# Optimization experiments

Hardware: AMD Instinct MI355X
Metric: run time of the kernel (lower is better)

## Reference

```python
import jax, jax.numpy as jnp
import numpy as np
from jax import lax

N_TAPS = 27  # 3x3x3 kernel

def _gather_one(xb, ti, hi, wi):
    # xb: (C,T,H,W); ti/hi/wi: (T,H,W) int32. Zero-fill outside bounds.
    C, T, H, W = xb.shape
    valid = (ti >= 0) & (ti < T) & (hi >= 0) & (hi < H) & (wi >= 0) & (wi < W)
    lin = (jnp.clip(ti, 0, T - 1) * H + jnp.clip(hi, 0, H - 1)) * W + jnp.clip(wi, 0, W - 1)
    v = jnp.take(xb.reshape(C, -1), lin.reshape(-1), axis=1).reshape(C, T, H, W)
    return v * valid.astype(xb.dtype)

_gather = jax.vmap(_gather_one)  # over batch

def _trilinear(x, t, h, w):
    # x: (B,C,T,H,W); t/h/w: (B,T,H,W) float sample coordinates.
    t0, h0, w0 = jnp.floor(t), jnp.floor(h), jnp.floor(w)
    lt, lh, lw = t - t0, h - h0, w - w0
    t0i, h0i, w0i = t0.astype(jnp.int32), h0.astype(jnp.int32), w0.astype(jnp.int32)
    acc = 0.0
    for ti, wt in ((t0i, 1.0 - lt), (t0i + 1, lt)):
        for hi, wh in ((h0i, 1.0 - lh), (h0i + 1, lh)):
            for wi, ww in ((w0i, 1.0 - lw), (w0i + 1, lw)):
                acc = acc + _gather(x, ti, hi, wi) * (wt * wh * ww)[:, None]
    return acc  # (B,C,T,H,W)

def _deform_conv3d(x, offset_w, offset_b, weight):
    # x: (B,Cin,T,H,W). Offset layout: (B, 3, 27, T, H, W), axis1=(dt,dh,dw),
    # tap index k = kt*9 + kh*3 + kw. stride=1, padding=1, dilation=1, no bias.
    off = lax.conv_general_dilated(
        x, offset_w, (1, 1, 1), [(1, 1)] * 3,
        dimension_numbers=("NCDHW", "OIDHW", "NCDHW"))
    off = off + offset_b[None, :, None, None, None]
    B, _, T, H, W = off.shape
    off = off.reshape(B, 3, N_TAPS, T, H, W)
    tg = jnp.arange(T, dtype=x.dtype)[:, None, None]
    hg = jnp.arange(H, dtype=x.dtype)[None, :, None]
    wg = jnp.arange(W, dtype=x.dtype)[None, None, :]
    out = jnp.zeros((B, weight.shape[0], T, H, W), x.dtype)
    for k in range(N_TAPS):
        kt, kh, kw = k // 9, (k // 3) % 3, k % 3
        t = tg + (kt - 1) + off[:, 0, k]
        h = hg + (kh - 1) + off[:, 1, k]
        w = wg + (kw - 1) + off[:, 2, k]
        s = _trilinear(x, t, h, w)  # (B,Cin,T,H,W)
        out = out + jnp.einsum('bcthw,oc->bothw', s, weight[:, :, kt, kh, kw])
    return out

def setup_inputs() -> dict:
    key = jax.random.key(0)
    ks = jax.random.split(key, 4)
    B, T, C, H, W = 1, 4, 64, 128, 128
    x = jax.random.normal(ks[0], (B, T, C, H, W), jnp.float32)
    # small init scale keeps predicted offsets in a realistic +-2px range
    offset_w = jax.random.normal(ks[1], (3 * N_TAPS, C, 3, 3, 3), jnp.float32) * 0.02
    offset_b = jnp.zeros((3 * N_TAPS,), jnp.float32)
    weight = jax.random.normal(ks[2], (C, C, 3, 3, 3), jnp.float32) * 0.02
    gamma = jax.random.normal(ks[3], (1,), jnp.float32) * 0.1
    return {"x": x, "offset_w": offset_w, "offset_b": offset_b,
            "weight": weight, "gamma": gamma}

def reference(x, offset_w, offset_b, weight, gamma):
    xp = jnp.transpose(x, (0, 2, 1, 3, 4))  # (B,C,T,H,W)
    xc = _deform_conv3d(xp, offset_w, offset_b, weight)
    return gamma[0] * jnp.transpose(xc, (0, 2, 1, 3, 4)) + x
```

## Files before the change

kernel.cpp:

```cpp
#include <hip/hip_runtime.h>
#include <cmath>

#define Cc 64
#define Hh 128
#define Ww 128
#define HW_ 16384
#define THW_ 65536
#define CHW_ 1048576
#define NT 27

typedef unsigned short ushort_t;
typedef _Float16 f16x2 __attribute__((ext_vector_type(2)));
typedef _Float16 f16x8 __attribute__((ext_vector_type(8)));
typedef __fp16 fp16x2_alt __attribute__((ext_vector_type(2)));
typedef float floatx4 __attribute__((ext_vector_type(4)));

union U32H2 { unsigned u; f16x2 h; };

static __device__ inline ushort_t f2h(float f) {
  union { _Float16 h; ushort_t u; } v;
  v.h = (_Float16)f;
  return v.u;
}

static __device__ inline unsigned pk2(float a) {
  union { fp16x2_alt h; unsigned u; } v;
  v.h = __builtin_amdgcn_cvt_pkrtz(a, a);
  return v.u;
}

#if defined(__has_builtin)
#if __has_builtin(__builtin_amdgcn_make_buffer_rsrc) && __has_builtin(__builtin_amdgcn_raw_buffer_load_b32)
#define USE_BUF 1
#endif
#endif
#ifndef USE_BUF
#define USE_BUF 0
#endif

struct XtBuf {
#if USE_BUF
  __amdgpu_buffer_rsrc_t r;
#else
  const unsigned* p;
#endif
};

static __device__ inline XtBuf mkbuf(const ushort_t* xt) {
  XtBuf b;
#if USE_BUF
  b.r = __builtin_amdgcn_make_buffer_rsrc((void*)xt, (short)0, 8388608, 0x00020000);
#else
  b.p = (const unsigned*)xt;
#endif
  return b;
}

static __device__ inline unsigned xload(const XtBuf& b, unsigned voff) {
#if USE_BUF
  return (unsigned)__builtin_amdgcn_raw_buffer_load_b32(b.r, (int)voff, 0, 0);
#else
  return b.p[voff >> 2];
#endif
}


__global__ __launch_bounds__(256) void prep(
    const float* __restrict__ offset_w,
    const float* __restrict__ weight,
    ushort_t* __restrict__ w2frag,
    ushort_t* __restrict__ wfrag)
{
  int e = blockIdx.x * 256 + threadIdx.x;
  if (e < 165888) {
    int j = e & 7, ln = (e >> 3) & 63, kh2 = (e >> 9) & 1, r = e >> 10;
    int ot = r % 6, k = r / 6;
    int oc = ot * 16 + (ln & 15);
    int c  = kh2 * 32 + (ln >> 4) * 8 + j;
    float v = (oc < 81) ? offset_w[(oc * 64 + c) * 27 + k] : 0.f;
    w2frag[e] = f2h(v);
  }
  if (e < 110592) {
    int j = e & 7, ln = (e >> 3) & 63, kh2 = (e >> 9) & 1, r = e >> 10;
    int ot = r & 3, k = r >> 2;
    int o = ot * 16 + (ln & 15);
    int c = kh2 * 32 + (ln >> 4) * 8 + j;
    wfrag[e] = f2h(weight[(o * 64 + c) * 27 + k]);
  }
}

__global__ __launch_bounds__(256) void transpose_x(
    const float* __restrict__ x, ushort_t* __restrict__ xt)
{
  __shared__ float tile[64][65];
  int b = blockIdx.x;
  int wblk = b & 1;
  int th = b >> 1;
  int h = th & 127;
  int t = th >> 7;
  int w0 = wblk * 64;
  int lane = threadIdx.x & 63;
  int quad = threadIdx.x >> 6;
  #pragma unroll
  for (int cc = 0; cc < 16; ++cc) {
    int c = cc * 4 + quad;
    tile[c][lane] = x[t * CHW_ + c * HW_ + h * Ww + w0 + lane];
  }
  __syncthreads();
  #pragma unroll
  for (int ww = 0; ww < 16; ++ww) {
    int w = ww * 4 + quad;
    xt[(size_t)(t * HW_ + h * Ww + w0 + w) * 64 + lane] = f2h(tile[lane][w]);
  }
}

__global__ __launch_bounds__(256) void offconv(
    const ushort_t* __restrict__ xt,
    const ushort_t* __restrict__ w2frag,
    const float* __restrict__ ob,
    float* __restrict__ off)
{
  __shared__ __align__(16) char lds[24960];
  ushort_t* S = (ushort_t*)lds;
  float* Dbuf = (float*)lds;
  int lane = threadIdx.x & 63;
  int wavei = __builtin_amdgcn_readfirstlane(threadIdx.x >> 6);
  int quad = lane >> 4;
  int m16 = lane & 15;
  int hlf = lane >> 5;
  int lo4 = (lane & 31) * 4;
  int p0 = blockIdx.x * 64;
  int t = p0 >> 14;
  int h = (p0 >> 7) & 127;
  int w0 = p0 & 127;
  XtBuf xb = mkbuf(xt);

  floatx4 acc[6];
  #pragma unroll
  for (int i = 0; i < 6; ++i) acc[i] = (floatx4){0.f, 0.f, 0.f, 0.f};

  for (int k = 0; k < NT; ++k) {
    int kt = k / 9, kh = (k / 3) % 3, kw = k % 3;
    int ts = t + kt - 1;
    int hs = h + kh - 1;
    bool rowok = ((unsigned)ts < 4u) && ((unsigned)hs < 128u);
    if (!rowok) continue;
    int sbase = ts * HW_ + hs * Ww;
    #pragma unroll
    for (int j = 0; j < 8; ++j) {
      int prow = wavei * 16 + j * 2 + hlf;
      int wc = w0 + prow + kw - 1;
      bool ok = (unsigned)wc < 128u;
      int wcc = min(max(wc, 0), 127);
      unsigned voff = ((unsigned)(sbase + wcc) << 7) + lo4;
      unsigned d = xload(xb, voff);
      d = ok ? d : 0u;
      *(unsigned*)((char*)S + prow * 144 + lo4) = d;
    }
    const ushort_t* srow = S + (wavei * 16 + m16) * 72 + quad * 8;
    f16x8 af0 = *(const f16x8*)srow;
    f16x8 af1 = *(const f16x8*)(srow + 32);
    #pragma unroll
    for (int ot = 0; ot < 6; ++ot) {
      const ushort_t* wb = w2frag + (size_t)((k * 6 + ot) * 2) * 512 + lane * 8;
      f16x8 b0 = *(const f16x8*)(wb);
      f16x8 b1 = *(const f16x8*)(wb + 512);
      acc[ot] = __builtin_amdgcn_mfma_f32_16x16x32_f16(af0, b0, acc[ot], 0, 0, 0);
      acc[ot] = __builtin_amdgcn_mfma_f32_16x16x32_f16(af1, b1, acc[ot], 0, 0, 0);
    }
  }
  __syncthreads();
  #pragma unroll
  for (int ot = 0; ot < 6; ++ot)
    #pragma unroll
    for (int r = 0; r < 4; ++r)
      Dbuf[(ot * 16 + m16) * 65 + wavei * 16 + quad * 4 + r] = acc[ot][r];
  __syncthreads();
  for (int i = threadIdx.x; i < 81 * 64; i += 256) {
    int oc = i >> 6, p = i & 63;
    off[(size_t)oc * THW_ + p0 + p] = Dbuf[oc * 65 + p] + ob[oc];
  }
}

__global__ __launch_bounds__(256) void deform(
    const float* __restrict__ x,
    const ushort_t* __restrict__ xt,
    const float* __restrict__ off,
    const ushort_t* __restrict__ wfrag,
    const float* __restrict__ gamma,
    float* __restrict__ out)
{
  __shared__ __align__(16) char lds[16640];
  ushort_t* S = (ushort_t*)lds;
  unsigned* meta = (unsigned*)(lds + 9216);
  float* Dbuf = (float*)lds;
  int lane = threadIdx.x & 63;
  int wavei = __builtin_amdgcn_readfirstlane(threadIdx.x >> 6);
  int quad = lane >> 4;
  int m16 = lane & 15;
  int hlf = lane >> 5;
  int lo4 = (lane & 31) * 4;
  int p0 = blockIdx.x * 64;
  int t = p0 >> 14;
  int h = (p0 >> 7) & 127;
  int w0 = p0 & 127;
  XtBuf xb = mkbuf(xt);

  floatx4 acc[4];
  #pragma unroll
  for (int i = 0; i < 4; ++i) acc[i] = (floatx4){0.f, 0.f, 0.f, 0.f};

  int pl = wavei * 16 + m16;
  int pm = p0 + pl;
  int aq = quad >> 1, bq = quad & 1;

  #pragma unroll 1
  for (int k = 0; k < NT; ++k) {
    int kt = k / 9, kh = (k / 3) % 3, kw = k % 3;
    float dt = off[(size_t)(0 * NT + k) * THW_ + pm];
    float dh = off[(size_t)(1 * NT + k) * THW_ + pm];
    float dw = off[(size_t)(2 * NT + k) * THW_ + pm];
    float tf = (float)(t + kt - 1) + dt;
    float hf = (float)(h + kh - 1) + dh;
    float wf = (float)(w0 + pl + kw - 1) + dw;
    float tF = floorf(tf), hF = floorf(hf), wF = floorf(wf);
    float lt = tf - tF, lh_ = hf - hF, lw_ = wf - wF;
    int t0 = (int)tF, h0 = (int)hF, wq_ = (int)wF;
    int ti = t0 + aq;
    float wt_ = (aq ? lt : 1.f - lt) * (((unsigned)ti < 4u) ? 1.f : 0.f);
    int tic = min(max(ti, 0), 3);
    int hi = h0 + bq;
    float wh_ = (bq ? lh_ : 1.f - lh_) * (((unsigned)hi < 128u) ? 1.f : 0.f);
    int hic = min(max(hi, 0), 127);
    int base2 = tic * HW_ + hic * Ww;
    float bw = wt_ * wh_;
    int wi0 = wq_;
    float ww0 = (1.f - lw_) * (((unsigned)wi0 < 128u) ? 1.f : 0.f);
    int wi0c = min(max(wi0, 0), 127);
    int wi1 = wq_ + 1;
    float ww1 = lw_ * (((unsigned)wi1 < 128u) ? 1.f : 0.f);
    int wi1c = min(max(wi1, 0), 127);
    uint4 me;
    me.x = (unsigned)(base2 + wi0c) << 7;
    me.y = pk2(bw * ww0);
    me.z = (unsigned)(base2 + wi1c) << 7;
    me.w = pk2(bw * ww1);
    *(uint4*)&meta[(pl * 8 + quad * 2) * 2] = me;

    #pragma unroll
    for (int j = 0; j < 8; ++j) {
      int prow = wavei * 16 + j * 2 + hlf;
      const uint4* mp = (const uint4*)&meta[prow * 16];
      uint4 c01 = mp[0], c23 = mp[1], c45 = mp[2], c67 = mp[3];
      U32H2 z; z.u = 0;
      f16x2 a2l = z.h, a2h = z.h;
      {
        unsigned d0 = xload(xb, c01.x + lo4);
        unsigned d1 = xload(xb, c01.z + lo4);
        unsigned d2 = xload(xb, c23.x + lo4);
        unsigned d3 = xload(xb, c23.z + lo4);
        unsigned d4 = xload(xb, c45.x + lo4);
        unsigned d5 = xload(xb, c45.z + lo4);
        unsigned d6 = xload(xb, c67.x + lo4);
        unsigned d7 = xload(xb, c67.z + lo4);
        U32H2 du, wu;
        du.u = d0; wu.u = c01.y; a2l += wu.h * du.h;
        du.u = d1; wu.u = c01.w; a2h += wu.h * du.h;
        du.u = d2; wu.u = c23.y; a2l += wu.h * du.h;
        du.u = d3; wu.u = c23.w; a2h += wu.h * du.h;
        du.u = d4; wu.u = c45.y; a2l += wu.h * du.h;
        du.u = d5; wu.u = c45.w; a2h += wu.h * du.h;
        du.u = d6; wu.u = c67.y; a2l += wu.h * du.h;
        du.u = d7; wu.u = c67.w; a2h += wu.h * du.h;
      }
      U32H2 res;
      res.h = a2l + a2h;
      *(unsigned*)((char*)S + prow * 144 + lo4) = res.u;
    }
    const ushort_t* srow = S + (wavei * 16 + m16) * 72 + quad * 8;
    f16x8 af0 = *(const f16x8*)srow;
    f16x8 af1 = *(const f16x8*)(srow + 32);
    #pragma unroll
    for (int ot = 0; ot < 4; ++ot) {
      const ushort_t* wb = wfrag + (size_t)((k * 4 + ot) * 2) * 512 + lane * 8;
      f16x8 b0 = *(const f16x8*)(wb);
      f16x8 b1 = *(const f16x8*)(wb + 512);
      acc[ot] = __builtin_amdgcn_mfma_f32_16x16x32_f16(af0, b0, acc[ot], 0, 0, 0);
      acc[ot] = __builtin_amdgcn_mfma_f32_16x16x32_f16(af1, b1, acc[ot], 0, 0, 0);
    }
  }
  __syncthreads();
  #pragma unroll
  for (int ot = 0; ot < 4; ++ot)
    #pragma unroll
    for (int r = 0; r < 4; ++r)
      Dbuf[(ot * 16 + m16) * 65 + wavei * 16 + quad * 4 + r] = acc[ot][r];
  __syncthreads();
  float g = gamma[0];
  for (int i = threadIdx.x; i < 64 * 64; i += 256) {
    int oc = i >> 6, p = i & 63;
    size_t oi = (size_t)t * CHW_ + (size_t)oc * HW_ + (size_t)h * Ww + w0 + p;
    out[oi] = fmaf(g, Dbuf[oc * 65 + p], x[oi]);
  }
}

extern "C" void kernel_launch(void* const* d_in, const int* in_sizes, int n_in,
                              void* d_out, int out_size, void* d_ws, size_t ws_size,
                              hipStream_t stream) {
  (void)in_sizes; (void)n_in; (void)out_size; (void)ws_size;
  const float* x        = (const float*)d_in[0];
  const float* offset_w = (const float*)d_in[1];
  const float* offset_b = (const float*)d_in[2];
  const float* weight   = (const float*)d_in[3];
  const float* gamma    = (const float*)d_in[4];
  float* out = (float*)d_out;
  float* wsf = (float*)d_ws;
  float*    off    = wsf;
  ushort_t* xt     = (ushort_t*)(wsf + 5308416);
  ushort_t* wfrag  = (ushort_t*)(wsf + 7405568);
  ushort_t* w2frag = (ushort_t*)(wsf + 7460864);

  hipLaunchKernelGGL(prep, dim3(648), dim3(256), 0, stream,
                     offset_w, weight, w2frag, wfrag);
  hipLaunchKernelGGL(transpose_x, dim3(1024), dim3(256), 0, stream, x, xt);
  hipLaunchKernelGGL(offconv, dim3(1024), dim3(256), 0, stream,
                     xt, w2frag, offset_b, off);
  hipLaunchKernelGGL(deform, dim3(1024), dim3(256), 0, stream,
                     x, xt, off, wfrag, gamma, out);
}
```

Before: 245.4 us.

## Software-pipeline gathers and offset loads, split metadata, batch all gather loads

In offconv, the next tap's 8 neighbour loads are issued into registers before the current tap's MFMAs run, and out-of-bounds rows are masked with clamped addresses instead of being skipped. In deform, the next tap's offsets are prefetched one iteration ahead. The LDS metadata is split into separate site and weight arrays so that all 64 gather loads per thread can be issued before any FMA consumes them. Both kernels get a launch bound of 4 blocks per CU, which raises register pressure (64 gather registers) and risks spills or lower occupancy in exchange for more memory-level parallelism.

```diff
diff --git a/kernel.cpp b/kernel.cpp
--- a/kernel.cpp
+++ b/kernel.cpp
@@ -114,7 +114,7 @@
   }
 }
 
-__global__ __launch_bounds__(256) void offconv(
+__global__ __launch_bounds__(256, 4) void offconv(
     const ushort_t* __restrict__ xt,
     const ushort_t* __restrict__ w2frag,
     const float* __restrict__ ob,
@@ -139,24 +139,37 @@
   #pragma unroll
   for (int i = 0; i < 6; ++i) acc[i] = (floatx4){0.f, 0.f, 0.f, 0.f};
 
-  for (int k = 0; k < NT; ++k) {
+  unsigned pd[8];
+
+  auto issue = [&](int k) {
     int kt = k / 9, kh = (k / 3) % 3, kw = k % 3;
-    int ts = t + kt - 1;
-    int hs = h + kh - 1;
-    bool rowok = ((unsigned)ts < 4u) && ((unsigned)hs < 128u);
-    if (!rowok) continue;
-    int sbase = ts * HW_ + hs * Ww;
+    int ts = t + kt - 1, hs = h + kh - 1;
+    int tsc = min(max(ts, 0), 3);
+    int hsc = min(max(hs, 0), 127);
+    int sbase = tsc * HW_ + hsc * Ww;
     #pragma unroll
     for (int j = 0; j < 8; ++j) {
       int prow = wavei * 16 + j * 2 + hlf;
       int wc = w0 + prow + kw - 1;
-      bool ok = (unsigned)wc < 128u;
       int wcc = min(max(wc, 0), 127);
-      unsigned voff = ((unsigned)(sbase + wcc) << 7) + lo4;
-      unsigned d = xload(xb, voff);
-      d = ok ? d : 0u;
-      *(unsigned*)((char*)S + prow * 144 + lo4) = d;
-    }
+      pd[j] = xload(xb, ((unsigned)(sbase + wcc) << 7) + lo4);
+    }
+  };
+
+  issue(0);
+  #pragma unroll 1
+  for (int k = 0; k < NT; ++k) {
+    int kt = k / 9, kh = (k / 3) % 3, kw = k % 3;
+    int ts = t + kt - 1, hs = h + kh - 1;
+    bool rowok = ((unsigned)ts < 4u) && ((unsigned)hs < 128u);
+    #pragma unroll
+    for (int j = 0; j < 8; ++j) {
+      int prow = wavei * 16 + j * 2 + hlf;
+      int wc = w0 + prow + kw - 1;
+      bool ok = rowok && ((unsigned)wc < 128u);
+      *(unsigned*)((char*)S + prow * 144 + lo4) = ok ? pd[j] : 0u;
+    }
+    issue(k + 1 < NT ? k + 1 : NT - 1);
     const ushort_t* srow = S + (wavei * 16 + m16) * 72 + quad * 8;
     f16x8 af0 = *(const f16x8*)srow;
     f16x8 af1 = *(const f16x8*)(srow + 32);
@@ -182,7 +195,7 @@
   }
 }
 
-__global__ __launch_bounds__(256) void deform(
+__global__ __launch_bounds__(256, 4) void deform(
     const float* __restrict__ x,
     const ushort_t* __restrict__ xt,
     const float* __restrict__ off,
@@ -192,7 +205,8 @@
 {
   __shared__ __align__(16) char lds[16640];
   ushort_t* S = (ushort_t*)lds;
-  unsigned* meta = (unsigned*)(lds + 9216);
+  unsigned* msite = (unsigned*)(lds + 9216);
+  unsigned* mwt   = (unsigned*)(lds + 11264);
   float* Dbuf = (float*)lds;
   int lane = threadIdx.x & 63;
   int wavei = __builtin_amdgcn_readfirstlane(threadIdx.x >> 6);
@@ -213,16 +227,23 @@
   int pl = wavei * 16 + m16;
   int pm = p0 + pl;
   int aq = quad >> 1, bq = quad & 1;
+  const float* offT = off + pm;
+
+  float dt_c = offT[(size_t)(0 * NT + 0) * THW_];
+  float dh_c = offT[(size_t)(1 * NT + 0) * THW_];
+  float dw_c = offT[(size_t)(2 * NT + 0) * THW_];
 
   #pragma unroll 1
   for (int k = 0; k < NT; ++k) {
+    int kn = (k + 1 < NT) ? k + 1 : NT - 1;
+    float dt_n = offT[(size_t)(0 * NT + kn) * THW_];
+    float dh_n = offT[(size_t)(1 * NT + kn) * THW_];
+    float dw_n = offT[(size_t)(2 * NT + kn) * THW_];
+
     int kt = k / 9, kh = (k / 3) % 3, kw = k % 3;
-    float dt = off[(size_t)(0 * NT + k) * THW_ + pm];
-    float dh = off[(size_t)(1 * NT + k) * THW_ + pm];
-    float dw = off[(size_t)(2 * NT + k) * THW_ + pm];
-    float tf = (float)(t + kt - 1) + dt;
-    float hf = (float)(h + kh - 1) + dh;
-    float wf = (float)(w0 + pl + kw - 1) + dw;
+    float tf = (float)(t + kt - 1) + dt_c;
+    float hf = (float)(h + kh - 1) + dh_c;
+    float wf = (float)(w0 + pl + kw - 1) + dw_c;
     float tF = floorf(tf), hF = floorf(hf), wF = floorf(wf);
     float lt = tf - tF, lh_ = hf - hF, lw_ = wf - wF;
     int t0 = (int)tF, h0 = (int)hF, wq_ = (int)wF;
@@ -240,39 +261,46 @@
     int wi1 = wq_ + 1;
     float ww1 = lw_ * (((unsigned)wi1 < 128u) ? 1.f : 0.f);
     int wi1c = min(max(wi1, 0), 127);
-    uint4 me;
-    me.x = (unsigned)(base2 + wi0c) << 7;
-    me.y = pk2(bw * ww0);
-    me.z = (unsigned)(base2 + wi1c) << 7;
-    me.w = pk2(bw * ww1);
-    *(uint4*)&meta[(pl * 8 + quad * 2) * 2] = me;
-
+    uint2 sp_;
+    sp_.x = (unsigned)(base2 + wi0c) << 7;
+    sp_.y = (unsigned)(base2 + wi1c) << 7;
+    *(uint2*)&msite[pl * 8 + quad * 2] = sp_;
+    uint2 wp_;
+    wp_.x = pk2(bw * ww0);
+    wp_.y = pk2(bw * ww1);
+    *(uint2*)&mwt[pl * 8 + quad * 2] = wp_;
+
+    unsigned dreg[8][8];
     #pragma unroll
     for (int j = 0; j < 8; ++j) {
       int prow = wavei * 16 + j * 2 + hlf;
-      const uint4* mp = (const uint4*)&meta[prow * 16];
-      uint4 c01 = mp[0], c23 = mp[1], c45 = mp[2], c67 = mp[3];
+      const uint4* spp = (const uint4*)&msite[prow * 8];
+      uint4 s03 = spp[0], s47 = spp[1];
+      dreg[j][0] = xload(xb, s03.x + lo4);
+      dreg[j][1] = xload(xb, s03.y + lo4);
+      dreg[j][2] = xload(xb, s03.z + lo4);
+      dreg[j][3] = xload(xb, s03.w + lo4);
+      dreg[j][4] = xload(xb, s47.x + lo4);
+      dreg[j][5] = xload(xb, s47.y + lo4);
+      dreg[j][6] = xload(xb, s47.z + lo4);
+      dreg[j][7] = xload(xb, s47.w + lo4);
+    }
+    #pragma unroll
+    for (int j = 0; j < 8; ++j) {
+      int prow = wavei * 16 + j * 2 + hlf;
+      const uint4* wpp = (const uint4*)&mwt[prow * 8];
+      uint4 w03 = wpp[0], w47 = wpp[1];
       U32H2 z; z.u = 0;
       f16x2 a2l = z.h, a2h = z.h;
-      {
-        unsigned d0 = xload(xb, c01.x + lo4);
-        unsigned d1 = xload(xb, c01.z + lo4);
-        unsigned d2 = xload(xb, c23.x + lo4);
-        unsigned d3 = xload(xb, c23.z + lo4);
-        unsigned d4 = xload(xb, c45.x + lo4);
-        unsigned d5 = xload(xb, c45.z + lo4);
-        unsigned d6 = xload(xb, c67.x + lo4);
-        unsigned d7 = xload(xb, c67.z + lo4);
-        U32H2 du, wu;
-        du.u = d0; wu.u = c01.y; a2l += wu.h * du.h;
-        du.u = d1; wu.u = c01.w; a2h += wu.h * du.h;
-        du.u = d2; wu.u = c23.y; a2l += wu.h * du.h;
-        du.u = d3; wu.u = c23.w; a2h += wu.h * du.h;
-        du.u = d4; wu.u = c45.y; a2l += wu.h * du.h;
-        du.u = d5; wu.u = c45.w; a2h += wu.h * du.h;
-        du.u = d6; wu.u = c67.y; a2l += wu.h * du.h;
-        du.u = d7; wu.u = c67.w; a2h += wu.h * du.h;
-      }
+      U32H2 du, wu;
+      du.u = dreg[j][0]; wu.u = w03.x; a2l += wu.h * du.h;
+      du.u = dreg[j][1]; wu.u = w03.y; a2h += wu.h * du.h;
+      du.u = dreg[j][2]; wu.u = w03.z; a2l += wu.h * du.h;
+      du.u = dreg[j][3]; wu.u = w03.w; a2h += wu.h * du.h;
+      du.u = dreg[j][4]; wu.u = w47.x; a2l += wu.h * du.h;
+      du.u = dreg[j][5]; wu.u = w47.y; a2h += wu.h * du.h;
+      du.u = dreg[j][6]; wu.u = w47.z; a2l += wu.h * du.h;
+      du.u = dreg[j][7]; wu.u = w47.w; a2h += wu.h * du.h;
       U32H2 res;
       res.h = a2l + a2h;
       *(unsigned*)((char*)S + prow * 144 + lo4) = res.u;
@@ -288,6 +316,7 @@
       acc[ot] = __builtin_amdgcn_mfma_f32_16x16x32_f16(af0, b0, acc[ot], 0, 0, 0);
       acc[ot] = __builtin_amdgcn_mfma_f32_16x16x32_f16(af1, b1, acc[ot], 0, 0, 0);
     }
+    dt_c = dt_n; dh_c = dh_n; dw_c = dw_n;
   }
   __syncthreads();
   #pragma unroll
```

Measured after the change: 227.7 us. -7.2%, faster.
